# Kernel tuning notes

Hardware: AMD Instinct MI355X
Metric: run time of the kernel (lower is better)

Reference implementation:

```python
import jax, jax.numpy as jnp
import numpy as np


def _gat(x, adj, W, a):
    # x: [N, J, Fin], W: [H, Fin, hs], a: [H, 2*hs]
    # e_ij = leakyrelu(a1.Wh_i + a2.Wh_j)  (decomposed form of the repeat/cat construction)
    hs = W.shape[-1]
    Wh = jnp.einsum('bjf,hfd->bhjd', x, W)
    s1 = jnp.einsum('bhjd,hd->bhj', Wh, a[:, :hs])
    s2 = jnp.einsum('bhjd,hd->bhj', Wh, a[:, hs:])
    e = jax.nn.leaky_relu(s1[..., :, None] + s2[..., None, :], 0.2)
    e = jnp.where(adj[None, None] > 0, e, jnp.float32(-9e15))
    att = jax.nn.softmax(e, axis=-1)
    h = jnp.einsum('bhij,bhjd->bhid', att, Wh)
    b, H, j, d = h.shape
    return jax.nn.elu(h.transpose(0, 2, 1, 3).reshape(b, j, H * d))


def _conv_bn_relu(x, w, bias, g, be, m, v):
    # x: [N, C, T], w: [O, I, 3], BN in inference mode
    y = jax.lax.conv_general_dilated(x, w, (1,), [(1, 1)], dimension_numbers=('NCH', 'OIH', 'NCH'))
    y = y + bias[None, :, None]
    y = (y - m[None, :, None]) / jnp.sqrt(v[None, :, None] + 1e-5) * g[None, :, None] + be[None, :, None]
    return jax.nn.relu(y)


def _mha(q, k, v, wq, bq, wk, bk, wv, bv, wo, bo):
    # torch nn.MultiheadAttention, 4 heads, eval mode (no dropout)
    n, L, D = q.shape
    H = 4
    hd = D // H
    def proj(x, w, b):
        return (x @ w.T + b).reshape(n, -1, H, hd)
    Q, K, V = proj(q, wq, bq), proj(k, wk, bk), proj(v, wv, bv)
    att = jax.nn.softmax(jnp.einsum('nqhd,nkhd->nhqk', Q, K) * jnp.float32(1.0 / np.sqrt(hd)), axis=-1)
    o = jnp.einsum('nhqk,nkhd->nqhd', att, V).reshape(n, L, D)
    return o @ wo.T + bo


def _lstm_dir(x, wih, whh, bih, bhh, rev):
    # x: [B, T, D]; torch gate order i, f, g, o
    b, t, _ = x.shape
    H = whh.shape[1]
    xw = jnp.transpose(x @ wih.T + (bih + bhh), (1, 0, 2))  # [T, B, 4H]
    def step(carry, xt):
        h, c = carry
        gates = xt + h @ whh.T
        i, f, g, o = jnp.split(gates, 4, axis=-1)
        c = jax.nn.sigmoid(f) * c + jax.nn.sigmoid(i) * jnp.tanh(g)
        h = jax.nn.sigmoid(o) * jnp.tanh(c)
        return (h, c), h
    init = (jnp.zeros((b, H), x.dtype), jnp.zeros((b, H), x.dtype))
    _, hs = jax.lax.scan(step, init, xw, reverse=rev)
    return jnp.transpose(hs, (1, 0, 2))


def _forward(lh, rh, adj, vis, g1W, g1a, g2W, g2a, c1w, c1b, b1g, b1b, b1m, b1v, c2w, c2b, b2g, b2b, b2m, b2v,
             wq, bq, wk, bk, wv, bv, wo, bo,
             l0fw, l0fu, l0fbi, l0fbh, l0bw, l0bu, l0bbi, l0bbh,
             l1fw, l1fu, l1fbi, l1fbh, l1bw, l1bu, l1bbi, l1bbh,
             o1w, o1b, o2w, o2b):
    B, T, J, F = lh.shape

    def single_hand(x):
        h = x.reshape(B * T, J, F)
        h = _gat(h, adj, g1W, g1a)
        h = _gat(h, adj, g2W, g2a)
        D = h.shape[-1]
        ht = h.reshape(B, T, J, D).transpose(0, 2, 3, 1).reshape(B * J, D, T)
        ht = _conv_bn_relu(ht, c1w, c1b, b1g, b1b, b1m, b1v)
        ht = _conv_bn_relu(ht, c2w, c2b, b2g, b2b, b2m, b2v)
        return ht.reshape(B, J, D, T).transpose(0, 3, 1, 2)  # [B, T, J, D]

    l = single_hand(lh)
    r = single_hand(rh)
    D = l.shape[-1]
    lf = l.reshape(B * T, J, D)
    rf = r.reshape(B * T, J, D)
    a_l2r = _mha(lf, rf, rf, wq, bq, wk, bk, wv, bv, wo, bo)
    a_r2l = _mha(rf, lf, lf, wq, bq, wk, bk, wv, bv, wo, bo)
    # repair of shape-inconsistent torch reshape: pool joints before the seq LSTM
    le = (lf + 0.5 * a_r2l).reshape(B, T, J, D).mean(axis=2)
    re = (rf + 0.5 * a_l2r).reshape(B, T, J, D).mean(axis=2)

    def bilstm(x):
        h1 = jnp.concatenate([_lstm_dir(x, l0fw, l0fu, l0fbi, l0fbh, False),
                              _lstm_dir(x, l0bw, l0bu, l0bbi, l0bbh, True)], -1)
        return jnp.concatenate([_lstm_dir(h1, l1fw, l1fu, l1fbi, l1fbh, False),
                                _lstm_dir(h1, l1bw, l1bu, l1bbi, l1bbh, True)], -1)

    def head(x):
        y = jax.nn.relu(x @ o1w.T + o1b) @ o2w.T + o2b  # [B, T, 3*J]
        return y.reshape(B, T, J, 3)

    lp = head(bilstm(le)) * vis[..., None]
    rp = head(bilstm(re)) * vis[..., None]
    return lp, rp


def setup_inputs() -> dict:
    key = jax.random.key(0)
    ks = jax.random.split(key, 60)
    it = iter(range(60))
    B, T, J, F, D = 8, 512, 21, 512, 256
    def nrm(shape, s=0.05):
        return jax.random.normal(ks[next(it)], shape, jnp.float32) * s
    inp = {}
    inp['left_hand_feats'] = nrm((B, T, J, F), 1.0)
    inp['right_hand_feats'] = nrm((B, T, J, F), 1.0)
    adj = (jax.random.uniform(ks[next(it)], (J, J)) < 0.3).astype(jnp.float32)
    inp['hand_adj_matrix'] = jnp.maximum(adj, jnp.eye(J, dtype=jnp.float32))
    inp['hand_visibility'] = jax.random.uniform(ks[next(it)], (B, T, J), jnp.float32)
    inp['gat1_W'] = nrm((4, F, 64)); inp['gat1_a'] = nrm((4, 128))
    inp['gat2_W'] = nrm((4, D, 64)); inp['gat2_a'] = nrm((4, 128))
    inp['conv1_w'] = nrm((D, D, 3)); inp['conv1_b'] = nrm((D,))
    inp['conv2_w'] = nrm((D, D, 3)); inp['conv2_b'] = nrm((D,))
    for p in ['bn1', 'bn2']:
        inp[p + '_g'] = jnp.ones((D,), jnp.float32)
        inp[p + '_b'] = jnp.zeros((D,), jnp.float32)
        inp[p + '_m'] = jnp.zeros((D,), jnp.float32)
        inp[p + '_v'] = jnp.ones((D,), jnp.float32)
    for p in ['attn_wq', 'attn_wk', 'attn_wv', 'attn_wo']:
        inp[p] = nrm((D, D))
    for p in ['attn_bq', 'attn_bk', 'attn_bv', 'attn_bo']:
        inp[p] = nrm((D,))
    H = D // 2
    for l in ['lstm0f', 'lstm0b', 'lstm1f', 'lstm1b']:
        inp[l + '_wih'] = nrm((4 * H, D))
        inp[l + '_whh'] = nrm((4 * H, H))
        inp[l + '_bih'] = nrm((4 * H,))
        inp[l + '_bhh'] = nrm((4 * H,))
    inp['out1_w'] = nrm((D, D)); inp['out1_b'] = nrm((D,))
    inp['out2_w'] = nrm((3 * J, D)); inp['out2_b'] = nrm((3 * J,))
    return inp


def reference(left_hand_feats, right_hand_feats, hand_adj_matrix, hand_visibility,
              gat1_W, gat1_a, gat2_W, gat2_a,
              conv1_w, conv1_b, bn1_g, bn1_b, bn1_m, bn1_v,
              conv2_w, conv2_b, bn2_g, bn2_b, bn2_m, bn2_v,
              attn_wq, attn_bq, attn_wk, attn_bk, attn_wv, attn_bv, attn_wo, attn_bo,
              lstm0f_wih, lstm0f_whh, lstm0f_bih, lstm0f_bhh,
              lstm0b_wih, lstm0b_whh, lstm0b_bih, lstm0b_bhh,
              lstm1f_wih, lstm1f_whh, lstm1f_bih, lstm1f_bhh,
              lstm1b_wih, lstm1b_whh, lstm1b_bih, lstm1b_bhh,
              out1_w, out1_b, out2_w, out2_b):
    return _forward(left_hand_feats, right_hand_feats, hand_adj_matrix, hand_visibility,
                    gat1_W, gat1_a, gat2_W, gat2_a,
                    conv1_w, conv1_b, bn1_g, bn1_b, bn1_m, bn1_v,
                    conv2_w, conv2_b, bn2_g, bn2_b, bn2_m, bn2_v,
                    attn_wq, attn_bq, attn_wk, attn_bk, attn_wv, attn_bv, attn_wo, attn_bo,
                    lstm0f_wih, lstm0f_whh, lstm0f_bih, lstm0f_bhh,
                    lstm0b_wih, lstm0b_whh, lstm0b_bih, lstm0b_bhh,
                    lstm1f_wih, lstm1f_whh, lstm1f_bih, lstm1f_bhh,
                    lstm1b_wih, lstm1b_whh, lstm1b_bih, lstm1b_bhh,
                    out1_w, out1_b, out2_w, out2_b)
```

## Files before the change

kernel.cpp:

```cpp
#include <hip/hip_runtime.h>

typedef __bf16 bf16;
typedef bf16 bf16x8 __attribute__((ext_vector_type(8)));
typedef float f32x4 __attribute__((ext_vector_type(4)));
typedef _Float16 f16;
typedef f16 f16x8 __attribute__((ext_vector_type(8)));

#define NBT 4096
#define NJ 21
#define NLF 86016
#define DD 256
#define CONV_M 86352
#define SPAD 514
#define CROWS 86528

__device__ __forceinline__ void gload16(const bf16* g, bf16* l) {
  __builtin_amdgcn_global_load_lds(
      (const __attribute__((address_space(1))) unsigned int*)g,
      (__attribute__((address_space(3))) unsigned int*)l, 16, 0, 0);
}

__global__ __launch_bounds__(256, 2) void gemm_bf16(
    const void* __restrict__ Av, const bf16* __restrict__ Bt,
    float* __restrict__ C32, bf16* __restrict__ Cout,
    const float* __restrict__ bias, const float* __restrict__ sc,
    const float* __restrict__ sh, int M, int N, int K, int lda, int flags)
{
  __shared__ __align__(16) bf16 As[128][32];
  __shared__ __align__(16) bf16 Bs[128][32];
  const int tid = threadIdx.x;
  const long m0 = (long)blockIdx.y * 128;
  const int n0 = blockIdx.x * 128;
  const int wave = tid >> 6, lane = tid & 63;
  const int wm = (wave & 1) * 64, wn = (wave >> 1) * 64;
  const int frow = lane & 15, fkb = (lane >> 4) * 8;
  const int crow = lane >> 2, ccol = (lane & 3) * 8;
  f32x4 acc[4][4] = {};
  for (int k0 = 0; k0 < K; k0 += 32) {
    if (flags & 1) {
      const int lr = tid >> 1, lc = (tid & 1) * 16;
      const float* ap = (const float*)Av + (m0 + lr) * (long)lda + (k0 + lc);
      bf16x8 t0, t1;
      #pragma unroll
      for (int u = 0; u < 8; u++) { t0[u] = (bf16)ap[u]; t1[u] = (bf16)ap[8 + u]; }
      *(bf16x8*)(&As[lr][lc])     = t0;
      *(bf16x8*)(&As[lr][lc + 8]) = t1;
    } else {
      #pragma unroll
      for (int cc = 0; cc < 2; cc++) {
        const int ch = wave * 2 + cc;
        gload16((const bf16*)Av + (m0 + ch * 16 + crow) * (long)lda + (k0 + ccol),
                &As[ch * 16][0]);
      }
    }
    #pragma unroll
    for (int cc = 0; cc < 2; cc++) {
      const int ch = wave * 2 + cc;
      gload16(Bt + (n0 + ch * 16 + crow) * (long)K + (k0 + ccol),
              &Bs[ch * 16][0]);
    }
    __syncthreads();
    bf16x8 af[4], bg[4];
    #pragma unroll
    for (int i = 0; i < 4; i++) af[i] = *(const bf16x8*)(&As[wm + i * 16 + frow][fkb]);
    #pragma unroll
    for (int j = 0; j < 4; j++) bg[j] = *(const bf16x8*)(&Bs[wn + j * 16 + frow][fkb]);
    #pragma unroll
    for (int i = 0; i < 4; i++)
      #pragma unroll
      for (int j = 0; j < 4; j++)
        acc[i][j] = __builtin_amdgcn_mfma_f32_16x16x32_bf16(af[i], bg[j], acc[i][j], 0, 0, 0);
    __syncthreads();
  }
  const int col = lane & 15, rbase = (lane >> 4) * 4;
  #pragma unroll
  for (int i = 0; i < 4; i++) {
    #pragma unroll
    for (int j = 0; j < 4; j++) {
      const int nn = n0 + wn + j * 16 + col;
      #pragma unroll
      for (int r = 0; r < 4; r++) {
        const long mm = m0 + wm + i * 16 + rbase + r;
        if (mm >= M) continue;
        float v = acc[i][j][r];
        if (flags & 2) { C32[mm * (long)N + nn] = v; continue; }
        if (flags & 8) v = v * sc[nn] + sh[nn];
        else if (bias) v += bias[nn];
        if (flags & 4) v = fmaxf(v, 0.f);
        if (flags & 16) {
          const int s = (int)(mm % SPAD);
          if (s == 0 || s == SPAD - 1) v = 0.f;
          Cout[mm * (long)N + nn] = (bf16)v;
        } else if (flags & 32) {
          const long hj = mm / SPAD; const int s = (int)(mm - hj * SPAD);
          if (s == 0 || s == SPAD - 1) continue;
          const long b = hj / NJ; const int j2 = (int)(hj - b * NJ);
          const long dst = (b * 512 + (s - 1)) * NJ + j2;
          Cout[dst * (long)N + nn] = (bf16)v;
        } else {
          Cout[mm * (long)N + nn] = (bf16)v;
        }
      }
    }
  }
}

__global__ void cvt_k(const float* __restrict__ s, bf16* __restrict__ d, long n) {
  long i = (long)blockIdx.x * 256 + threadIdx.x;
  if (i < n) d[i] = (bf16)s[i];
}
__global__ void prep_gatW(const float* __restrict__ W, bf16* __restrict__ Wt, int F) {
  long idx = (long)blockIdx.x * 256 + threadIdx.x;
  if (idx >= 256L * F) return;
  int n = (int)(idx / F), f = (int)(idx % F);
  Wt[idx] = (bf16)W[((long)(n >> 6) * F + f) * 64 + (n & 63)];
}
__global__ void prep_convw(const float* __restrict__ w, bf16* __restrict__ wp) {
  int idx = blockIdx.x * 256 + threadIdx.x;
  int n = idx / 768, k = idx % 768, tap = k >> 8, i = k & 255;
  wp[idx] = (bf16)w[(n * 256 + i) * 3 + tap];
}
__global__ void prep_out2(const float* __restrict__ w, bf16* __restrict__ wp) {
  int idx = blockIdx.x * 256 + threadIdx.x;
  wp[idx] = (idx < 63 * 256) ? (bf16)w[idx] : (bf16)0.f;
}
__global__ void prep_scsh(const float* __restrict__ cb, const float* __restrict__ g,
                          const float* __restrict__ be, const float* __restrict__ m,
                          const float* __restrict__ v, float* __restrict__ sc,
                          float* __restrict__ sh) {
  int c = threadIdx.x;
  float rs = rsqrtf(v[c] + 1e-5f) * g[c];
  sc[c] = rs; sh[c] = (cb[c] - m[c]) * rs + be[c];
}
__global__ void pad_zero(bf16* __restrict__ convIn) {
  int idx = blockIdx.x * 256 + threadIdx.x;
  int hj = idx >> 9, s = ((idx >> 8) & 1) ? (SPAD - 1) : 0, c = idx & 255;
  convIn[((long)hj * SPAD + s) * DD + c] = (bf16)0.f;
}
__global__ void zero_out(float* __restrict__ o, long n) {
  long i = (long)blockIdx.x * 256 + threadIdx.x;
  if (i < n) o[i] = 0.f;
}

__global__ __launch_bounds__(256) void gat_attn(
    const bf16* __restrict__ Wh, const float* __restrict__ a,
    const float* __restrict__ adj, bf16* __restrict__ out, int convMode)
{
  const int bt = blockIdx.x, tid = threadIdx.x;
  __shared__ float whs[NJ][DD];
  __shared__ float s1[4][NJ], s2[4][NJ];
  __shared__ float att[4][NJ][NJ];
  const long base = (long)bt * NJ * DD;
  for (int i = tid; i < NJ * DD; i += 256)
    whs[i >> 8][i & 255] = (float)Wh[base + i];
  __syncthreads();
  if (tid < 4 * NJ) {
    const int h = tid / NJ, i = tid % NJ;
    float x1 = 0.f, x2 = 0.f;
    for (int d = 0; d < 64; d++) {
      const float w = whs[i][h * 64 + d];
      x1 += w * a[h * 128 + d];
      x2 += w * a[h * 128 + 64 + d];
    }
    s1[h][i] = x1; s2[h][i] = x2;
  }
  __syncthreads();
  for (int idx = tid; idx < 4 * NJ * NJ; idx += 256) {
    const int h = idx / (NJ * NJ), r = idx % (NJ * NJ), i = r / NJ, j = r % NJ;
    float e = s1[h][i] + s2[h][j];
    e = e > 0.f ? e : 0.2f * e;
    att[h][i][j] = (adj[i * NJ + j] > 0.f) ? e : -9e15f;
  }
  __syncthreads();
  if (tid < 4 * NJ) {
    const int h = tid / NJ, i = tid % NJ;
    float mx = -3e38f;
    for (int j = 0; j < NJ; j++) mx = fmaxf(mx, att[h][i][j]);
    float sum = 0.f;
    for (int j = 0; j < NJ; j++) { const float ex = __expf(att[h][i][j] - mx); att[h][i][j] = ex; sum += ex; }
    const float inv = 1.f / sum;
    for (int j = 0; j < NJ; j++) att[h][i][j] *= inv;
  }
  __syncthreads();
  const int b = bt >> 9, t = bt & 511;
  for (int idx = tid; idx < NJ * DD; idx += 256) {
    const int i = idx >> 8, c = idx & 255, h = c >> 6;
    float s = 0.f;
    for (int j = 0; j < NJ; j++) s += att[h][i][j] * whs[j][c];
    s = s > 0.f ? s : (__expf(s) - 1.f);
    const long row = convMode ? (((long)(b * NJ + i)) * SPAD + (t + 1)) : ((long)bt * NJ + i);
    out[row * DD + c] = (bf16)s;
  }
}

__global__ __launch_bounds__(256) void mha_core(
    const bf16* __restrict__ Q, const bf16* __restrict__ K,
    const bf16* __restrict__ V, bf16* __restrict__ O)
{
  const int bt = blockIdx.x, tid = threadIdx.x;
  __shared__ bf16 qs[NJ][DD], ks[NJ][DD], vs[NJ][DD];
  __shared__ float att[4][NJ][NJ];
  const long base = (long)bt * NJ * DD;
  for (int i = tid; i < NJ * DD; i += 256) {
    const int r = i >> 8, c = i & 255;
    qs[r][c] = Q[base + i]; ks[r][c] = K[base + i]; vs[r][c] = V[base + i];
  }
  __syncthreads();
  for (int idx = tid; idx < 4 * NJ * NJ; idx += 256) {
    const int h = idx / (NJ * NJ), r = idx % (NJ * NJ), i = r / NJ, j = r % NJ;
    float s = 0.f;
    for (int d = 0; d < 64; d++) s += (float)qs[i][h * 64 + d] * (float)ks[j][h * 64 + d];
    att[h][i][j] = s * 0.125f;
  }
  __syncthreads();
  if (tid < 4 * NJ) {
    const int h = tid / NJ, i = tid % NJ;
    float mx = -3e38f;
    for (int j = 0; j < NJ; j++) mx = fmaxf(mx, att[h][i][j]);
    float sum = 0.f;
    for (int j = 0; j < NJ; j++) { const float ex = __expf(att[h][i][j] - mx); att[h][i][j] = ex; sum += ex; }
    const float inv = 1.f / sum;
    for (int j = 0; j < NJ; j++) att[h][i][j] *= inv;
  }
  __syncthreads();
  for (int idx = tid; idx < NJ * DD; idx += 256) {
    const int i = idx >> 8, c = idx & 255, h = c >> 6;
    float s = 0.f;
    for (int j = 0; j < NJ; j++) s += att[h][i][j] * (float)vs[j][c];
    O[base + i * DD + c] = (bf16)s;
  }
}

__global__ __launch_bounds__(256) void pool_kernel(
    const bf16* __restrict__ lf, const bf16* __restrict__ ao, bf16* __restrict__ o)
{
  const int bt = blockIdx.x, c = threadIdx.x;
  float s = 0.f;
  for (int j = 0; j < NJ; j++) {
    const long r = ((long)bt * NJ + j) * DD + c;
    s += (float)lf[r] + 0.5f * (float)ao[r];
  }
  o[(long)bt * DD + c] = (bf16)(s * (1.f / 21.f));
}

#define REP16(X) X(0) X(1) X(2) X(3) X(4) X(5) X(6) X(7) X(8) X(9) X(10) X(11) \
  X(12) X(13) X(14) X(15)

#define LDS_FENCE() do { \
  asm volatile("s_waitcnt lgkmcnt(0)" ::: "memory"); \
  __builtin_amdgcn_sched_barrier(0); \
  __builtin_amdgcn_s_barrier(); \
  __builtin_amdgcn_sched_barrier(0); \
} while (0)

__global__ __launch_bounds__(512, 1) void lstm_lds(
    const float* __restrict__ xw,
    const float* __restrict__ whhF, const float* __restrict__ whhB,
    const float* __restrict__ bihF, const float* __restrict__ bhhF,
    const float* __restrict__ bihB, const float* __restrict__ bhhB,
    bf16* __restrict__ outL, bf16* __restrict__ outR)
{
  const int wg = blockIdx.x;
  const int hand = wg >> 4, dir = (wg >> 3) & 1, b = wg & 7;
  const int tid = threadIdx.x;
  const float* whh = dir ? whhB : whhF;

  __shared__ f16 whhs[512][136];
  __shared__ f16 hbuf[136];
  __shared__ float gsb[512];

  for (int i = tid; i < 512 * 128; i += 512)
    whhs[i >> 7][i & 127] = (f16)whh[i];
  if (tid < 136) hbuf[tid] = (f16)0.f;
  const float bias = (dir ? bihB : bihF)[tid] + (dir ? bhhB : bhhF)[tid];
  float c = 0.f;
  const float* xp = xw + (((long)(hand * 2 + dir)) * NBT + (long)b * 512) * 512;
  bf16* outp = hand ? outR : outL;
  float xv = xp[(long)(dir ? 511 : 0) * 512 + tid];
  __syncthreads();

  const f16* wrow = &whhs[tid][0];
#define WRD(i) f16x8 w##i = *(const f16x8*)(wrow + (i) * 8);
  REP16(WRD)
#undef WRD

  for (int s = 0; s < 512; s++) {
    const int t = dir ? (511 - s) : s;
    const int tn = dir ? (510 - s) : (s + 1);
    float xnext = 0.f;
    if (s < 511) xnext = xp[(long)tn * 512 + tid];
    float a0 = xv + bias, a1 = 0.f, a2 = 0.f, a3 = 0.f;
#define WDOT(i) { \
    const f16x8 hv = *(const f16x8*)(&hbuf[(i) * 8]); \
    a0 = __builtin_amdgcn_fdot2(__builtin_shufflevector(w##i, w##i, 0, 1), \
                                __builtin_shufflevector(hv, hv, 0, 1), a0, false); \
    a1 = __builtin_amdgcn_fdot2(__builtin_shufflevector(w##i, w##i, 2, 3), \
                                __builtin_shufflevector(hv, hv, 2, 3), a1, false); \
    a2 = __builtin_amdgcn_fdot2(__builtin_shufflevector(w##i, w##i, 4, 5), \
                                __builtin_shufflevector(hv, hv, 4, 5), a2, false); \
    a3 = __builtin_amdgcn_fdot2(__builtin_shufflevector(w##i, w##i, 6, 7), \
                                __builtin_shufflevector(hv, hv, 6, 7), a3, false); }
    REP16(WDOT)
#undef WDOT
    gsb[tid] = (a0 + a1) + (a2 + a3);
    LDS_FENCE();
    if (tid < 128) {
      const float ig = gsb[tid], fg = gsb[tid + 128], gg = gsb[tid + 256], og = gsb[tid + 384];
      const float si = __builtin_amdgcn_rcpf(1.f + __expf(-ig));
      const float sf = __builtin_amdgcn_rcpf(1.f + __expf(-fg));
      const float so = __builtin_amdgcn_rcpf(1.f + __expf(-og));
      const float tg = 1.f - 2.f * __builtin_amdgcn_rcpf(1.f + __expf(2.f * gg));
      c = sf * c + si * tg;
      const float tc = 1.f - 2.f * __builtin_amdgcn_rcpf(1.f + __expf(2.f * c));
      const float h = so * tc;
      hbuf[tid] = (f16)h;
      outp[((long)b * 512 + t) * 256 + dir * 128 + tid] = (bf16)h;
    }
    LDS_FENCE();
    xv = xnext;
  }
}

__global__ __launch_bounds__(256) void finalize_k(
    const float* __restrict__ y, const float* __restrict__ b2,
    const float* __restrict__ vis, float* __restrict__ out)
{
  const int idx = blockIdx.x * 256 + threadIdx.x;
  if (idx >= NBT * 63) return;
  const int c = idx % 63; const int bt = idx / 63;
  out[idx] = (y[(long)bt * 128 + c] + b2[c]) * vis[bt * 21 + (c / 3)];
}

extern "C" void kernel_launch(void* const* d_in, const int* in_sizes, int n_in,
                              void* d_out, int out_size, void* d_ws, size_t ws_size,
                              hipStream_t stream) {
  (void)in_sizes; (void)n_in;
  const float* feats[2] = { (const float*)d_in[0], (const float*)d_in[1] };
  const float* adj  = (const float*)d_in[2];
  const float* vis  = (const float*)d_in[3];
  const float* gW[2] = { (const float*)d_in[4], (const float*)d_in[6] };
  const float* ga[2] = { (const float*)d_in[5], (const float*)d_in[7] };
  const float* cw_[2] = { (const float*)d_in[8],  (const float*)d_in[10] };
  const float* cb_[2] = { (const float*)d_in[9],  (const float*)d_in[11] };
  const float* bng[2] = { (const float*)d_in[12], (const float*)d_in[16] };
  const float* bnb[2] = { (const float*)d_in[13], (const float*)d_in[17] };
  const float* bnm[2] = { (const float*)d_in[14], (const float*)d_in[18] };
  const float* bnv[2] = { (const float*)d_in[15], (const float*)d_in[19] };
  const float* wq = (const float*)d_in[20], *wk = (const float*)d_in[21];
  const float* wv = (const float*)d_in[22], *wo = (const float*)d_in[23];
  const float* bq = (const float*)d_in[24], *bk = (const float*)d_in[25];
  const float* bv = (const float*)d_in[26], *bo = (const float*)d_in[27];
  const float* Lwih[2][2] = { { (const float*)d_in[28], (const float*)d_in[32] },
                              { (const float*)d_in[36], (const float*)d_in[40] } };
  const float* Lwhh[2][2] = { { (const float*)d_in[29], (const float*)d_in[33] },
                              { (const float*)d_in[37], (const float*)d_in[41] } };
  const float* Lbih[2][2] = { { (const float*)d_in[30], (const float*)d_in[34] },
                              { (const float*)d_in[38], (const float*)d_in[42] } };
  const float* Lbhh[2][2] = { { (const float*)d_in[31], (const float*)d_in[35] },
                              { (const float*)d_in[39], (const float*)d_in[43] } };
  const float* o1w = (const float*)d_in[44], *o1b = (const float*)d_in[45];
  const float* o2w = (const float*)d_in[46], *o2b = (const float*)d_in[47];

  char* base = (char*)d_ws;
  size_t off = 0;
  auto alloc = [&](size_t b) { size_t r = off; off += (b + 1023) & ~(size_t)1023; return r; };
  const size_t SZ_LF  = (size_t)NLF * DD * 2;
  const size_t SZ_CNV = (size_t)CROWS * DD * 2;
  const size_t SZ_BT  = (size_t)NBT * DD * 2;
  const size_t o_w1t = alloc((size_t)256 * 512 * 2);
  const size_t o_w2t = alloc((size_t)256 * 256 * 2);
  const size_t o_cw1 = alloc((size_t)256 * 768 * 2);
  const size_t o_cw2 = alloc((size_t)256 * 768 * 2);
  const size_t o_wq  = alloc((size_t)256 * 256 * 2);
  const size_t o_wk  = alloc((size_t)256 * 256 * 2);
  const size_t o_wv  = alloc((size_t)256 * 256 * 2);
  const size_t o_wo  = alloc((size_t)256 * 256 * 2);
  const size_t o_o1w = alloc((size_t)256 * 256 * 2);
  const size_t o_o2p = alloc((size_t)128 * 256 * 2);
  const size_t o_lw0 = alloc((size_t)512 * 256 * 2);
  const size_t o_lw1 = alloc((size_t)512 * 256 * 2);
  const size_t o_lw2 = alloc((size_t)512 * 256 * 2);
  const size_t o_lw3 = alloc((size_t)512 * 256 * 2);
  const size_t o_ss  = alloc((size_t)4 * 256 * 4);
  const size_t o_B1  = alloc(SZ_LF);
  const size_t o_B2  = alloc(SZ_CNV);
  const size_t o_B3  = alloc(SZ_CNV);
  const size_t o_lfL = alloc(SZ_LF);
  const size_t o_lfR = alloc(SZ_LF);
  const size_t o_le  = alloc(SZ_BT);
  const size_t o_re  = alloc(SZ_BT);
  const size_t o_h1L = alloc(SZ_BT);
  const size_t o_h1R = alloc(SZ_BT);
  const size_t o_hoL = alloc(SZ_BT);
  const size_t o_hoR = alloc(SZ_BT);
  const size_t o_t1  = alloc(SZ_BT);
  const size_t o_y32 = alloc((size_t)NBT * 128 * 4);
  const size_t NEED = off;
  if (ws_size < NEED) {
    zero_out<<<(out_size + 255) / 256, 256, 0, stream>>>((float*)d_out, out_size);
    return;
  }
  auto P = [&](size_t o_) { return (void*)(base + o_); };

  auto gemm = [&](const void* A, const void* Bt, void* c32, void* co,
                  const void* bias_, const void* sc_, const void* sh_,
                  long M, int N, int K, int lda, int flags) {
    dim3 g((unsigned)(N / 128), (unsigned)((M + 127) / 128));
    gemm_bf16<<<g, 256, 0, stream>>>(A, (const bf16*)Bt, (float*)c32, (bf16*)co,
                                     (const float*)bias_, (const float*)sc_,
                                     (const float*)sh_, (int)M, N, K, lda, flags);
  };
  auto cvt = [&](const float* s, void* d, long n) {
    cvt_k<<<(unsigned)((n + 255) / 256), 256, 0, stream>>>(s, (bf16*)d, n);
  };

  prep_gatW<<<512, 256, 0, stream>>>(gW[0], (bf16*)P(o_w1t), 512);
  prep_gatW<<<256, 256, 0, stream>>>(gW[1], (bf16*)P(o_w2t), 256);
  prep_convw<<<768, 256, 0, stream>>>(cw_[0], (bf16*)P(o_cw1));
  prep_convw<<<768, 256, 0, stream>>>(cw_[1], (bf16*)P(o_cw2));
  cvt(wq, P(o_wq), 65536); cvt(wk, P(o_wk), 65536);
  cvt(wv, P(o_wv), 65536); cvt(wo, P(o_wo), 65536);
  cvt(o1w, P(o_o1w), 65536);
  cvt(Lwih[0][0], P(o_lw0), 131072); cvt(Lwih[0][1], P(o_lw1), 131072);
  cvt(Lwih[1][0], P(o_lw2), 131072); cvt(Lwih[1][1], P(o_lw3), 131072);
  prep_out2<<<128, 256, 0, stream>>>(o2w, (bf16*)P(o_o2p));
  float* sc1 = (float*)P(o_ss); float* sh1 = sc1 + 256;
  float* sc2 = sh1 + 256;       float* sh2 = sc2 + 256;
  prep_scsh<<<1, 256, 0, stream>>>(cb_[0], bng[0], bnb[0], bnm[0], bnv[0], sc1, sh1);
  prep_scsh<<<1, 256, 0, stream>>>(cb_[1], bng[1], bnb[1], bnm[1], bnv[1], sc2, sh2);

  bf16* B1 = (bf16*)P(o_B1);
  bf16* B2 = (bf16*)P(o_B2);
  bf16* B3 = (bf16*)P(o_B3);
  bf16* lfb[2] = { (bf16*)P(o_lfL), (bf16*)P(o_lfR) };

  for (int hd = 0; hd < 2; hd++) {
    gemm(feats[hd], P(o_w1t), nullptr, B1, nullptr, nullptr, nullptr,
         NLF, 256, 512, 512, 1);
    gat_attn<<<NBT, 256, 0, stream>>>(B1, ga[0], adj, B1, 0);
    gemm(B1, P(o_w2t), nullptr, B2, nullptr, nullptr, nullptr,
         NLF, 256, 256, 256, 0);
    pad_zero<<<336, 256, 0, stream>>>(B3 + DD);
    gat_attn<<<NBT, 256, 0, stream>>>(B2, ga[1], adj, B3 + DD, 1);
    gemm(B3, P(o_cw1), nullptr, B2 + DD, nullptr, sc1, sh1,
         CONV_M, 256, 768, 256, 8 | 4 | 16);
    gemm(B2, P(o_cw2), nullptr, lfb[hd], nullptr, sc2, sh2,
         CONV_M, 256, 768, 256, 8 | 4 | 32);
  }

  gemm(lfb[0], P(o_wq), nullptr, B1, bq, nullptr, nullptr, NLF, 256, 256, 256, 0);
  gemm(lfb[1], P(o_wk), nullptr, B2, bk, nullptr, nullptr, NLF, 256, 256, 256, 0);
  gemm(lfb[1], P(o_wv), nullptr, B3, bv, nullptr, nullptr, NLF, 256, 256, 256, 0);
  mha_core<<<NBT, 256, 0, stream>>>(B1, B2, B3, B1);
  gemm(B1, P(o_wo), nullptr, B2, bo, nullptr, nullptr, NLF, 256, 256, 256, 0);
  pool_kernel<<<NBT, 256, 0, stream>>>(lfb[1], B2, (bf16*)P(o_re));
  gemm(lfb[1], P(o_wq), nullptr, B1, bq, nullptr, nullptr, NLF, 256, 256, 256, 0);
  gemm(lfb[0], P(o_wk), nullptr, B3, bk, nullptr, nullptr, NLF, 256, 256, 256, 0);
  gemm(lfb[0], P(o_wv), nullptr, B2, bv, nullptr, nullptr, NLF, 256, 256, 256, 0);
  mha_core<<<NBT, 256, 0, stream>>>(B1, B3, B2, B1);
  gemm(B1, P(o_wo), nullptr, B3, bo, nullptr, nullptr, NLF, 256, 256, 256, 0);
  pool_kernel<<<NBT, 256, 0, stream>>>(lfb[0], B3, (bf16*)P(o_le));

  float* xw = (float*)P(o_B2);
  auto xslot = [&](int h_, int d_) { return (void*)(xw + ((size_t)(h_ * 2 + d_)) * NBT * 512); };
  gemm(P(o_le), P(o_lw0), xslot(0, 0), nullptr, nullptr, nullptr, nullptr, NBT, 512, 256, 256, 2);
  gemm(P(o_le), P(o_lw1), xslot(0, 1), nullptr, nullptr, nullptr, nullptr, NBT, 512, 256, 256, 2);
  gemm(P(o_re), P(o_lw0), xslot(1, 0), nullptr, nullptr, nullptr, nullptr, NBT, 512, 256, 256, 2);
  gemm(P(o_re), P(o_lw1), xslot(1, 1), nullptr, nullptr, nullptr, nullptr, NBT, 512, 256, 256, 2);
  lstm_lds<<<32, 512, 0, stream>>>(xw, Lwhh[0][0], Lwhh[0][1],
      Lbih[0][0], Lbhh[0][0], Lbih[0][1], Lbhh[0][1],
      (bf16*)P(o_h1L), (bf16*)P(o_h1R));
  gemm(P(o_h1L), P(o_lw2), xslot(0, 0), nullptr, nullptr, nullptr, nullptr, NBT, 512, 256, 256, 2);
  gemm(P(o_h1L), P(o_lw3), xslot(0, 1), nullptr, nullptr, nullptr, nullptr, NBT, 512, 256, 256, 2);
  gemm(P(o_h1R), P(o_lw2), xslot(1, 0), nullptr, nullptr, nullptr, nullptr, NBT, 512, 256, 256, 2);
  gemm(P(o_h1R), P(o_lw3), xslot(1, 1), nullptr, nullptr, nullptr, nullptr, NBT, 512, 256, 256, 2);
  lstm_lds<<<32, 512, 0, stream>>>(xw, Lwhh[1][0], Lwhh[1][1],
      Lbih[1][0], Lbhh[1][0], Lbih[1][1], Lbhh[1][1],
      (bf16*)P(o_hoL), (bf16*)P(o_hoR));

  for (int hd = 0; hd < 2; hd++) {
    const void* hin = hd ? P(o_hoR) : P(o_hoL);
    gemm(hin, P(o_o1w), nullptr, P(o_t1), o1b, nullptr, nullptr, NBT, 256, 256, 256, 4);
    gemm(P(o_t1), P(o_o2p), P(o_y32), nullptr, nullptr, nullptr, nullptr, NBT, 128, 256, 256, 2);
    finalize_k<<<(NBT * 63 + 255) / 256, 256, 0, stream>>>(
        (const float*)P(o_y32), o2b, vis, (float*)d_out + (size_t)hd * NBT * 63);
  }
}
```

Measured before the change: 2.337 ms.

## Merge LSTM input-projection GEMMs, pre-convert features to bf16, pin LSTM weights in AGPRs

Measured after the change: 2.511 ms. 1.07x slower.

```diff
diff --git a/kernel.cpp b/kernel.cpp
--- a/kernel.cpp
+++ b/kernel.cpp
@@ -2,6 +2,7 @@
 
 typedef __bf16 bf16;
 typedef bf16 bf16x8 __attribute__((ext_vector_type(8)));
+typedef bf16 bf16x4 __attribute__((ext_vector_type(4)));
 typedef float f32x4 __attribute__((ext_vector_type(4)));
 typedef _Float16 f16;
 typedef f16 f16x8 __attribute__((ext_vector_type(8)));
@@ -109,6 +110,13 @@
   long i = (long)blockIdx.x * 256 + threadIdx.x;
   if (i < n) d[i] = (bf16)s[i];
 }
+__global__ void cvt4_k(const float* __restrict__ s, bf16* __restrict__ d, long n4) {
+  long i = (long)blockIdx.x * 256 + threadIdx.x;
+  if (i >= n4) return;
+  const f32x4 v = ((const f32x4*)s)[i];
+  bf16x4 o; o[0] = (bf16)v[0]; o[1] = (bf16)v[1]; o[2] = (bf16)v[2]; o[3] = (bf16)v[3];
+  ((bf16x4*)d)[i] = o;
+}
 __global__ void prep_gatW(const float* __restrict__ W, bf16* __restrict__ Wt, int F) {
   long idx = (long)blockIdx.x * 256 + threadIdx.x;
   if (idx >= 256L * F) return;
@@ -274,21 +282,28 @@
   if (tid < 136) hbuf[tid] = (f16)0.f;
   const float bias = (dir ? bihB : bihF)[tid] + (dir ? bhhB : bhhF)[tid];
   float c = 0.f;
-  const float* xp = xw + (((long)(hand * 2 + dir)) * NBT + (long)b * 512) * 512;
+  const float* xp = xw + ((long)hand * NBT + (long)b * 512) * 1024 + dir * 512;
   bf16* outp = hand ? outR : outL;
-  float xv = xp[(long)(dir ? 511 : 0) * 512 + tid];
+  float xv = xp[(long)(dir ? 511 : 0) * 1024 + tid];
   __syncthreads();
 
   const f16* wrow = &whhs[tid][0];
 #define WRD(i) f16x8 w##i = *(const f16x8*)(wrow + (i) * 8);
   REP16(WRD)
 #undef WRD
+  asm volatile("" : "+a"(w0), "+a"(w1), "+a"(w2), "+a"(w3));
+  asm volatile("" : "+a"(w4), "+a"(w5), "+a"(w6), "+a"(w7));
+  asm volatile("" : "+a"(w8), "+a"(w9), "+a"(w10), "+a"(w11));
+  asm volatile("" : "+a"(w12), "+a"(w13), "+a"(w14), "+a"(w15));
 
   for (int s = 0; s < 512; s++) {
+#define WKEEP(i) asm volatile("" : "+a"(w##i));
+    REP16(WKEEP)
+#undef WKEEP
     const int t = dir ? (511 - s) : s;
     const int tn = dir ? (510 - s) : (s + 1);
     float xnext = 0.f;
-    if (s < 511) xnext = xp[(long)tn * 512 + tid];
+    if (s < 511) xnext = xp[(long)tn * 1024 + tid];
     float a0 = xv + bias, a1 = 0.f, a2 = 0.f, a3 = 0.f;
 #define WDOT(i) { \
     const f16x8 hv = *(const f16x8*)(&hbuf[(i) * 8]); \
@@ -383,8 +398,7 @@
   const size_t o_lw3 = alloc((size_t)512 * 256 * 2);
   const size_t o_ss  = alloc((size_t)4 * 256 * 4);
   const size_t o_B1  = alloc(SZ_LF);
-  const size_t o_B2  = alloc(SZ_CNV);
-  const size_t o_B3  = alloc(SZ_CNV);
+  const size_t o_B23 = alloc(2 * SZ_CNV);
   const size_t o_lfL = alloc(SZ_LF);
   const size_t o_lfR = alloc(SZ_LF);
   const size_t o_le  = alloc(SZ_BT);
@@ -430,13 +444,16 @@
   prep_scsh<<<1, 256, 0, stream>>>(cb_[1], bng[1], bnb[1], bnm[1], bnv[1], sc2, sh2);
 
   bf16* B1 = (bf16*)P(o_B1);
-  bf16* B2 = (bf16*)P(o_B2);
-  bf16* B3 = (bf16*)P(o_B3);
+  bf16* B2 = (bf16*)P(o_B23);
+  bf16* B3 = B2 + (size_t)CROWS * DD;
   bf16* lfb[2] = { (bf16*)P(o_lfL), (bf16*)P(o_lfR) };
 
   for (int hd = 0; hd < 2; hd++) {
-    gemm(feats[hd], P(o_w1t), nullptr, B1, nullptr, nullptr, nullptr,
-         NLF, 256, 512, 512, 1);
+    bf16* featbf = B2;
+    cvt4_k<<<(unsigned)(((long)NLF * 512 / 4 + 255) / 256), 256, 0, stream>>>(
+        feats[hd], featbf, (long)NLF * 512 / 4);
+    gemm(featbf, P(o_w1t), nullptr, B1, nullptr, nullptr, nullptr,
+         NLF, 256, 512, 512, 0);
     gat_attn<<<NBT, 256, 0, stream>>>(B1, ga[0], adj, B1, 0);
     gemm(B1, P(o_w2t), nullptr, B2, nullptr, nullptr, nullptr,
          NLF, 256, 256, 256, 0);
@@ -461,19 +478,14 @@
   gemm(B1, P(o_wo), nullptr, B3, bo, nullptr, nullptr, NLF, 256, 256, 256, 0);
   pool_kernel<<<NBT, 256, 0, stream>>>(lfb[0], B3, (bf16*)P(o_le));
 
-  float* xw = (float*)P(o_B2);
-  auto xslot = [&](int h_, int d_) { return (void*)(xw + ((size_t)(h_ * 2 + d_)) * NBT * 512); };
-  gemm(P(o_le), P(o_lw0), xslot(0, 0), nullptr, nullptr, nullptr, nullptr, NBT, 512, 256, 256, 2);
-  gemm(P(o_le), P(o_lw1), xslot(0, 1), nullptr, nullptr, nullptr, nullptr, NBT, 512, 256, 256, 2);
-  gemm(P(o_re), P(o_lw0), xslot(1, 0), nullptr, nullptr, nullptr, nullptr, NBT, 512, 256, 256, 2);
-  gemm(P(o_re), P(o_lw1), xslot(1, 1), nullptr, nullptr, nullptr, nullptr, NBT, 512, 256, 256, 2);
+  float* xw = (float*)P(o_B23);
+  gemm(P(o_le), P(o_lw0), xw,                    nullptr, nullptr, nullptr, nullptr, NBT, 1024, 256, 256, 2);
+  gemm(P(o_re), P(o_lw0), xw + (size_t)NBT * 1024, nullptr, nullptr, nullptr, nullptr, NBT, 1024, 256, 256, 2);
   lstm_lds<<<32, 512, 0, stream>>>(xw, Lwhh[0][0], Lwhh[0][1],
       Lbih[0][0], Lbhh[0][0], Lbih[0][1], Lbhh[0][1],
       (bf16*)P(o_h1L), (bf16*)P(o_h1R));
-  gemm(P(o_h1L), P(o_lw2), xslot(0, 0), nullptr, nullptr, nullptr, nullptr, NBT, 512, 256, 256, 2);
-  gemm(P(o_h1L), P(o_lw3), xslot(0, 1), nullptr, nullptr, nullptr, nullptr, NBT, 512, 256, 256, 2);
-  gemm(P(o_h1R), P(o_lw2), xslot(1, 0), nullptr, nullptr, nullptr, nullptr, NBT, 512, 256, 256, 2);
-  gemm(P(o_h1R), P(o_lw3), xslot(1, 1), nullptr, nullptr, nullptr, nullptr, NBT, 512, 256, 256, 2);
+  gemm(P(o_h1L), P(o_lw2), xw,                    nullptr, nullptr, nullptr, nullptr, NBT, 1024, 256, 256, 2);
+  gemm(P(o_h1R), P(o_lw2), xw + (size_t)NBT * 1024, nullptr, nullptr, nullptr, nullptr, NBT, 1024, 256, 256, 2);
   lstm_lds<<<32, 512, 0, stream>>>(xw, Lwhh[1][0], Lwhh[1][1],
       Lbih[1][0], Lbhh[1][0], Lbih[1][1], Lbhh[1][1],
       (bf16*)P(o_hoL), (bf16*)P(o_hoR));
```
